# Optimization experiments

Measured on AMD Instinct MI355X. Metric: run time of the kernel, lower is better.

## Reference

```python
import jax, jax.numpy as jnp
import numpy as np

NEG_SLOPE = 0.2
LN_EPS = 1e-5


def setup_inputs() -> dict:
    key = jax.random.key(0)
    k1, k2, k3, k4 = jax.random.split(key, 4)
    N, E, Din, Dout = 50000, 1000000, 64, 64
    h = jax.random.normal(k1, (N, Din), dtype=jnp.float32)
    edge_index = jax.random.randint(k2, (2, E), 0, N, dtype=jnp.int32)
    # Linear(in_dim, out_dim, bias=False): weight [Dout, Din]
    W = jax.random.normal(k3, (Dout, Din), dtype=jnp.float32) / np.sqrt(Din)
    # attention vector a: [1, 2*Dout] (xavier-normal-ish scale)
    a = jax.random.normal(k4, (1, 2 * Dout), dtype=jnp.float32) * 0.1
    ln_gamma = jnp.ones((Dout,), dtype=jnp.float32)
    ln_beta = jnp.zeros((Dout,), dtype=jnp.float32)
    return {"h": h, "edge_index": edge_index, "W": W, "a": a,
            "ln_gamma": ln_gamma, "ln_beta": ln_beta}


def reference(h, edge_index, W, a, ln_gamma, ln_beta):
    N, Dout = h.shape[0], W.shape[0]
    src, dst = edge_index[0], edge_index[1]
    hW = h @ W.T  # [N, Dout]
    # score_e = leakyrelu([h_src || h_dst] . a) = leakyrelu(s1[src] + s2[dst])
    a1, a2 = a[0, :Dout], a[0, Dout:]
    s1 = hW @ a1  # [N]
    s2 = hW @ a2  # [N]
    e = jax.nn.leaky_relu(s1[src] + s2[dst], NEG_SLOPE)  # [E]
    # softmax grouped by source node (segment softmax), numerically stable
    m = jax.ops.segment_max(e, src, num_segments=N)  # [N]
    ex = jnp.exp(e - m[src])
    denom = jax.ops.segment_sum(ex, src, num_segments=N)  # [N]
    att = ex / denom[src]  # [E]  (dropout: eval mode, identity)
    # scatter-add weighted source features into destination nodes
    msg = att[:, None] * hW[src]  # [E, Dout]
    h_prime = jnp.zeros_like(hW).at[dst].add(msg)
    # residual + LayerNorm
    x = hW + h_prime
    mu = jnp.mean(x, axis=-1, keepdims=True)
    var = jnp.var(x, axis=-1, keepdims=True)
    return (x - mu) * jax.lax.rsqrt(var + LN_EPS) * ln_gamma + ln_beta
```

## Files before the change

### kernel.cpp

```cpp
#include <hip/hip_runtime.h>
#include <hip/hip_bf16.h>

#define NEG_SLOPE 0.2f
#define LN_EPS 1e-5f
#define D 64
#define BSH 6
#define BNODES 64
#define NBMAX 1024
#define BCAP 1792
#define SSH 8
#define NSBMAX 256
#define SCAP 6144
#define OVFCAP 65536

typedef unsigned long long u64;
typedef unsigned int u32;
typedef unsigned short u16;

__device__ __forceinline__ u16 f2bf(float f) {
    u32 u = __float_as_uint(f);
    return (u16)((u + 0x7FFFu + ((u >> 16) & 1u)) >> 16);
}
__device__ __forceinline__ float bf_lo(u32 p) { return __uint_as_float(p << 16); }
__device__ __forceinline__ float bf_hi(u32 p) { return __uint_as_float(p & 0xFFFF0000u); }

__global__ void __launch_bounds__(256, 4)
k_hw_scores(const float* __restrict__ h,
            const float* __restrict__ W,
            const float* __restrict__ a,
            float* __restrict__ hW,
            u16* __restrict__ hWb,
            float* __restrict__ s1,
            float* __restrict__ s2,
            int N) {
    const int lane = threadIdx.x & 63;
    const int wid  = threadIdx.x >> 6;
    const int wavesPerBlock = blockDim.x >> 6;
    const int nWaves = gridDim.x * wavesPerBlock;

    float wcol[D];
    {
        const float4* wr = (const float4*)(W + (size_t)lane * D);
        #pragma unroll
        for (int q = 0; q < D / 4; ++q) {
            float4 w4 = wr[q];
            wcol[q * 4 + 0] = w4.x; wcol[q * 4 + 1] = w4.y;
            wcol[q * 4 + 2] = w4.z; wcol[q * 4 + 3] = w4.w;
        }
    }
    const float a1l = a[lane];
    const float a2l = a[D + lane];

    for (int i = blockIdx.x * wavesPerBlock + wid; i < N; i += nWaves) {
        const int iu = __builtin_amdgcn_readfirstlane(i);
        const float* hr = h + (size_t)iu * D;

        float acc0 = 0.f, acc1 = 0.f, acc2 = 0.f, acc3 = 0.f;
        #pragma unroll
        for (int k = 0; k < D; k += 4) {
            acc0 = fmaf(hr[k + 0], wcol[k + 0], acc0);
            acc1 = fmaf(hr[k + 1], wcol[k + 1], acc1);
            acc2 = fmaf(hr[k + 2], wcol[k + 2], acc2);
            acc3 = fmaf(hr[k + 3], wcol[k + 3], acc3);
        }
        float c = (acc0 + acc1) + (acc2 + acc3);
        hW[(size_t)iu * D + lane] = c;
        hWb[(size_t)iu * D + lane] = f2bf(c);

        float p1 = c * a1l;
        float p2 = c * a2l;
        #pragma unroll
        for (int off = 32; off > 0; off >>= 1) {
            p1 += __shfl_xor(p1, off, 64);
            p2 += __shfl_xor(p2, off, 64);
        }
        if (lane == 0) { s1[iu] = p1; s2[iu] = p2; }
    }
}

__device__ __forceinline__ float edge_ex(float v1, float v2) {
    float x = v1 + v2;
    float e = x > 0.f ? x : NEG_SLOPE * x;
    return expf(fminf(e, 60.f));
}

__global__ void __launch_bounds__(1024)
k_bin(const int* __restrict__ src,
      const int* __restrict__ dst,
      const float* __restrict__ s1,
      const float* __restrict__ s2,
      float* __restrict__ denom,
      int* __restrict__ dcnt_g,
      u32* __restrict__ drecs,
      int* __restrict__ scnt_g,
      u32* __restrict__ srecs,
      u32* __restrict__ ovf_rec,
      int* __restrict__ ovf_dst,
      int* __restrict__ ovf_n,
      int E, int nb, int nsb) {
    const int TPB = 1024, EPT = 4;
    __shared__ u32 recbuf[TPB * EPT];
    __shared__ int lcnt[NBMAX], lo[NBMAX], cc[NBMAX], lbase[NBMAX];

    const int tid = threadIdx.x;
    const int chunk = blockIdx.x * (TPB * EPT);
    const int total = min(E - chunk, TPB * EPT);

    int sv[EPT], dv[EPT];
    const int e0 = chunk + tid * EPT;
    if (e0 + EPT <= E) {
        int4 s4 = *(const int4*)(src + e0);
        int4 d4 = *(const int4*)(dst + e0);
        sv[0] = s4.x; sv[1] = s4.y; sv[2] = s4.z; sv[3] = s4.w;
        dv[0] = d4.x; dv[1] = d4.y; dv[2] = d4.z; dv[3] = d4.w;
    } else {
        #pragma unroll
        for (int j = 0; j < EPT; ++j) {
            int i = e0 + j;
            sv[j] = (i < E) ? src[i] : 0;
            dv[j] = (i < E) ? dst[i] : -1;
        }
    }

    for (int i = tid; i < nb; i += TPB) lcnt[i] = 0;
    __syncthreads();
    #pragma unroll
    for (int j = 0; j < EPT; ++j)
        if (dv[j] >= 0) atomicAdd(&lcnt[dv[j] >> BSH], 1);
    __syncthreads();

    if (tid < nb) lo[tid] = lcnt[tid];
    __syncthreads();
    for (int off = 1; off < nb; off <<= 1) {
        int t = 0;
        if (tid < nb && tid >= off) t = lo[tid - off];
        __syncthreads();
        if (tid < nb) lo[tid] += t;
        __syncthreads();
    }
    if (tid < nb) {
        int e_ = lo[tid] - lcnt[tid];
        lo[tid] = e_; cc[tid] = e_;
        if (lcnt[tid]) lbase[tid] = atomicAdd(&dcnt_g[tid], lcnt[tid]);
    }
    __syncthreads();

    #pragma unroll
    for (int j = 0; j < EPT; ++j) {
        if (dv[j] < 0) continue;
        int b = dv[j] >> BSH;
        u32 rec = (u32)sv[j] | ((u32)(dv[j] & (BNODES - 1)) << 16) | ((u32)b << 22);
        recbuf[atomicAdd(&cc[b], 1)] = rec;
    }
    __syncthreads();

    for (int i = tid; i < total; i += TPB) {
        u32 rec = recbuf[i];
        int b = rec >> 22;
        int r = lbase[b] + (i - lo[b]);
        if (r < BCAP) {
            drecs[(size_t)b * BCAP + r] = rec;
        } else {
            int o = atomicAdd(ovf_n, 1);
            if (o < OVFCAP) {
                ovf_rec[o] = rec;
                ovf_dst[o] = (b << BSH) | ((rec >> 16) & (BNODES - 1));
            }
        }
    }
    __syncthreads();

    for (int i = tid; i < nsb; i += TPB) lcnt[i] = 0;
    __syncthreads();
    #pragma unroll
    for (int j = 0; j < EPT; ++j)
        if (dv[j] >= 0) atomicAdd(&lcnt[sv[j] >> SSH], 1);
    __syncthreads();

    if (tid < nsb) lo[tid] = lcnt[tid];
    __syncthreads();
    for (int off = 1; off < nsb; off <<= 1) {
        int t = 0;
        if (tid < nsb && tid >= off) t = lo[tid - off];
        __syncthreads();
        if (tid < nsb) lo[tid] += t;
        __syncthreads();
    }
    if (tid < nsb) {
        int e_ = lo[tid] - lcnt[tid];
        lo[tid] = e_; cc[tid] = e_;
        if (lcnt[tid]) lbase[tid] = atomicAdd(&scnt_g[tid], lcnt[tid]);
    }
    __syncthreads();

    #pragma unroll
    for (int j = 0; j < EPT; ++j) {
        if (dv[j] < 0) continue;
        int b = sv[j] >> SSH;
        u32 rec = (u32)sv[j] | ((u32)dv[j] << 16);
        recbuf[atomicAdd(&cc[b], 1)] = rec;
    }
    __syncthreads();

    for (int i = tid; i < total; i += TPB) {
        u32 rec = recbuf[i];
        int s = rec & 0xFFFF;
        int b = s >> SSH;
        int r = lbase[b] + (i - lo[b]);
        if (r < SCAP) {
            srecs[(size_t)b * SCAP + r] = rec;
        } else {
            atomicAdd(&denom[s], edge_ex(s1[s], s2[rec >> 16]));
        }
    }
}

__global__ void __launch_bounds__(512)
k_denom(const u32* __restrict__ srecs,
        const int* __restrict__ scnt_g,
        const float* __restrict__ s1,
        const float* __restrict__ s2,
        float* __restrict__ denom,
        int N) {
    __shared__ float acc[256];
    const int b = blockIdx.x;
    const int tid = threadIdx.x;
    if (tid < 256) acc[tid] = 0.f;
    __syncthreads();

    const int total = min(scnt_g[b], SCAP);
    const u32* base = srecs + (size_t)b * SCAP;
    for (int i = tid; i < total; i += 512) {
        u32 r = base[i];
        int s = r & 0xFFFF;
        int d = r >> 16;
        atomicAdd(&acc[s & 255], edge_ex(s1[s], s2[d]));
    }
    __syncthreads();

    if (tid < 256) {
        int g = (b << SSH) + tid;
        if (g < N) denom[g] += acc[tid];
    }
}

__global__ void __launch_bounds__(512)
k_bucket_agg(const u32* __restrict__ drecs,
             const int* __restrict__ dcnt_g,
             const float* __restrict__ s1,
             const float* __restrict__ s2,
             const float* __restrict__ denom,
             const float* __restrict__ hW,
             const u16* __restrict__ hWb,
             const float* __restrict__ gamma,
             const float* __restrict__ beta,
             const u32* __restrict__ ovf_rec,
             const int* __restrict__ ovf_dst,
             const int* __restrict__ ovf_n_p,
             float* __restrict__ out,
             int N) {
    __shared__ u64 ro[BCAP];
    __shared__ float s2l[BNODES];
    __shared__ int hh[BNODES], oo[BNODES], cc[BNODES];

    const int b    = blockIdx.x;
    const int tid  = threadIdx.x;
    const int lane = tid & 63;
    const int wid  = tid >> 6;
    const int g    = lane >> 4;
    const int li   = lane & 15;
    const int node0 = b << BSH;
    const int nn    = min(BNODES, N - node0);
    const int total = min(dcnt_g[b], BCAP);

    if (tid < nn) s2l[tid] = s2[node0 + tid];
    if (tid < BNODES) hh[tid] = 0;
    __syncthreads();

    u64 rr[4]; bool valid[4];
    const u32* base = drecs + (size_t)b * BCAP;
    #pragma unroll
    for (int q = 0; q < 4; ++q) {
        int idx = tid + q * 512;
        valid[q] = idx < total;
        u32 r = valid[q] ? base[idx] : 0u;
        if (valid[q]) {
            int s  = r & 0xFFFF;
            int dl = (r >> 16) & (BNODES - 1);
            float att = edge_ex(s1[s], s2l[dl]) / denom[s];
            rr[q] = ((u64)__float_as_uint(att) << 32) | (u64)r;
            atomicAdd(&hh[dl], 1);
        } else rr[q] = 0;
    }
    __syncthreads();

    if (tid < BNODES) oo[tid] = hh[tid];
    __syncthreads();
    for (int off = 1; off < BNODES; off <<= 1) {
        int t = 0;
        if (tid < BNODES && tid >= off) t = oo[tid - off];
        __syncthreads();
        if (tid < BNODES) oo[tid] += t;
        __syncthreads();
    }
    if (tid < BNODES) { int e_ = oo[tid] - hh[tid]; oo[tid] = e_; cc[tid] = e_; }
    __syncthreads();

    #pragma unroll
    for (int q = 0; q < 4; ++q) if (valid[q])
        ro[atomicAdd(&cc[((u32)rr[q] >> 16) & (BNODES - 1)], 1)] = rr[q];
    __syncthreads();

    int ovn = *ovf_n_p;
    if (ovn > OVFCAP) ovn = OVFCAP;

    #pragma unroll
    for (int k = 0; k < 8; ++k) {
        int nl = (wid << 3) + k;
        if (nl >= nn) break;
        int beg = oo[nl], end = cc[nl];

        float ax = 0.f, ay = 0.f, az = 0.f, aw = 0.f;
        for (int p = beg; p < end; p += 16) {
            float at0 = 0.f, at1 = 0.f, at2 = 0.f, at3 = 0.f;
            int s0 = 0, s1i = 0, s2i = 0, s3 = 0;
            int i0 = p + g, i1 = p + 4 + g, i2 = p + 8 + g, i3 = p + 12 + g;
            if (i0 < end) { u64 r2 = ro[i0]; s0  = (u32)r2 & 0xFFFF; at0 = __uint_as_float((u32)(r2 >> 32)); }
            if (i1 < end) { u64 r2 = ro[i1]; s1i = (u32)r2 & 0xFFFF; at1 = __uint_as_float((u32)(r2 >> 32)); }
            if (i2 < end) { u64 r2 = ro[i2]; s2i = (u32)r2 & 0xFFFF; at2 = __uint_as_float((u32)(r2 >> 32)); }
            if (i3 < end) { u64 r2 = ro[i3]; s3  = (u32)r2 & 0xFFFF; at3 = __uint_as_float((u32)(r2 >> 32)); }
            const uint2 v0 = *(const uint2*)(hWb + (size_t)s0  * D + li * 4);
            const uint2 v1 = *(const uint2*)(hWb + (size_t)s1i * D + li * 4);
            const uint2 v2 = *(const uint2*)(hWb + (size_t)s2i * D + li * 4);
            const uint2 v3 = *(const uint2*)(hWb + (size_t)s3  * D + li * 4);
            ax = fmaf(at0, bf_lo(v0.x), ax); ay = fmaf(at0, bf_hi(v0.x), ay);
            az = fmaf(at0, bf_lo(v0.y), az); aw = fmaf(at0, bf_hi(v0.y), aw);
            ax = fmaf(at1, bf_lo(v1.x), ax); ay = fmaf(at1, bf_hi(v1.x), ay);
            az = fmaf(at1, bf_lo(v1.y), az); aw = fmaf(at1, bf_hi(v1.y), aw);
            ax = fmaf(at2, bf_lo(v2.x), ax); ay = fmaf(at2, bf_hi(v2.x), ay);
            az = fmaf(at2, bf_lo(v2.y), az); aw = fmaf(at2, bf_hi(v2.y), aw);
            ax = fmaf(at3, bf_lo(v3.x), ax); ay = fmaf(at3, bf_hi(v3.x), ay);
            az = fmaf(at3, bf_lo(v3.y), az); aw = fmaf(at3, bf_hi(v3.y), aw);
        }

        for (int r = 0; r < ovn; ++r) {
            if (ovf_dst[r] != node0 + nl) continue;
            if (g == 0) {
                u32 r2 = ovf_rec[r];
                int s = r2 & 0xFFFF;
                float att = edge_ex(s1[s], s2l[nl]) / denom[s];
                const uint2 v = *(const uint2*)(hWb + (size_t)s * D + li * 4);
                ax = fmaf(att, bf_lo(v.x), ax); ay = fmaf(att, bf_hi(v.x), ay);
                az = fmaf(att, bf_lo(v.y), az); aw = fmaf(att, bf_hi(v.y), aw);
            }
        }

        ax += __shfl_xor(ax, 16, 64); ax += __shfl_xor(ax, 32, 64);
        ay += __shfl_xor(ay, 16, 64); ay += __shfl_xor(ay, 32, 64);
        az += __shfl_xor(az, 16, 64); az += __shfl_xor(az, 32, 64);
        aw += __shfl_xor(aw, 16, 64); aw += __shfl_xor(aw, 32, 64);

        const float4 hv = *(const float4*)(hW + (size_t)(node0 + nl) * D + li * 4);
        float x0 = hv.x + ax, x1 = hv.y + ay, x2 = hv.z + az, x3 = hv.w + aw;

        float sm = x0 + x1 + x2 + x3;
        sm += __shfl_xor(sm, 1, 64); sm += __shfl_xor(sm, 2, 64);
        sm += __shfl_xor(sm, 4, 64); sm += __shfl_xor(sm, 8, 64);
        float mu = sm * (1.f / D);
        float d0 = x0 - mu, d1 = x1 - mu, d2 = x2 - mu, d3 = x3 - mu;
        float vv = d0 * d0 + d1 * d1 + d2 * d2 + d3 * d3;
        vv += __shfl_xor(vv, 1, 64); vv += __shfl_xor(vv, 2, 64);
        vv += __shfl_xor(vv, 4, 64); vv += __shfl_xor(vv, 8, 64);
        float inv = rsqrtf(vv * (1.f / D) + LN_EPS);

        if (g == 0) {
            const float4 gm = *(const float4*)(gamma + li * 4);
            const float4 bt = *(const float4*)(beta + li * 4);
            float4 o;
            o.x = d0 * inv * gm.x + bt.x;
            o.y = d1 * inv * gm.y + bt.y;
            o.z = d2 * inv * gm.z + bt.z;
            o.w = d3 * inv * gm.w + bt.w;
            *(float4*)(out + (size_t)(node0 + nl) * D + li * 4) = o;
        }
    }
}

static inline size_t align256(size_t x) { return (x + 255) & ~size_t(255); }

extern "C" void kernel_launch(void* const* d_in, const int* in_sizes, int n_in,
                              void* d_out, int out_size, void* d_ws, size_t ws_size,
                              hipStream_t stream) {
    const float* h    = (const float*)d_in[0];
    const int*   ei   = (const int*)d_in[1];
    const float* W    = (const float*)d_in[2];
    const float* a    = (const float*)d_in[3];
    const float* lng  = (const float*)d_in[4];
    const float* lnb  = (const float*)d_in[5];
    float* out = (float*)d_out;

    const int N = in_sizes[0] / D;
    const int E = in_sizes[1] / 2;
    const int* src = ei;
    const int* dst = ei + E;
    const int nb  = (N + BNODES - 1) >> BSH;
    const int nsb = (N + 255) >> SSH;

    char* ws = (char*)d_ws;
    size_t off = 0;
    float* hW      = (float*)(ws + off); off += align256(sizeof(float) * (size_t)N * D);
    u16*   hWb     = (u16*)  (ws + off); off += align256(sizeof(u16) * (size_t)N * D);
    float* s1      = (float*)(ws + off); off += align256(sizeof(float) * (size_t)N);
    float* s2      = (float*)(ws + off); off += align256(sizeof(float) * (size_t)N);
    u32*   drecs   = (u32*)  (ws + off); off += align256(sizeof(u32) * (size_t)nb * BCAP);
    u32*   srecs   = (u32*)  (ws + off); off += align256(sizeof(u32) * (size_t)nsb * SCAP);
    u32*   ovf_rec = (u32*)  (ws + off); off += align256(sizeof(u32) * (size_t)OVFCAP);
    int*   ovf_dst = (int*)  (ws + off); off += align256(sizeof(int) * (size_t)OVFCAP);
    size_t zero_off = off;
    float* denom   = (float*)(ws + off); off += align256(sizeof(float) * (size_t)N);
    int*   dcnt_g  = (int*)  (ws + off); off += align256(sizeof(int) * (size_t)NBMAX);
    int*   scnt_g  = (int*)  (ws + off); off += align256(sizeof(int) * (size_t)NSBMAX);
    int*   ovf_n   = (int*)  (ws + off); off += align256(sizeof(int));
    size_t zero_bytes = off - zero_off;

    hipMemsetAsync(ws + zero_off, 0, zero_bytes, stream);

    k_hw_scores<<<dim3(1024), dim3(256), 0, stream>>>(h, W, a, hW, hWb, s1, s2, N);

    k_bin<<<dim3((E + 4095) / 4096), dim3(1024), 0, stream>>>(
        src, dst, s1, s2, denom, dcnt_g, drecs, scnt_g, srecs,
        ovf_rec, ovf_dst, ovf_n, E, nb, nsb);

    k_denom<<<dim3(nsb), dim3(512), 0, stream>>>(srecs, scnt_g, s1, s2, denom, N);

    k_bucket_agg<<<dim3(nb), dim3(512), 0, stream>>>(
        drecs, dcnt_g, s1, s2, denom, hW, hWb, lng, lnb,
        ovf_rec, ovf_dst, ovf_n, out, N);
}
```

Before: 163.8 us.

## Fuse projection and edge binning into one kernel with block-role split

Merges the hW/score projection kernel and the edge binning kernel into a single launch, where the first blocks bin edges and the remaining 200 blocks compute hW and scores concurrently. Because binning no longer has s1/s2 available, source-bucket overflow edges are written to a new overflow list that k_denom scans, instead of being atomically added into denom. k_denom now writes denom directly. This removes a kernel boundary and overlaps the compute-light projection with the atomic-heavy binning. In exchange, the projection blocks run with 1024 threads and hold a 64-float register array, which limits occupancy, and every k_denom block scans the whole overflow list.

Result: no change. 165.0 us (+0.7%).

```diff
diff --git a/kernel.cpp b/kernel.cpp
--- a/kernel.cpp
+++ b/kernel.cpp
@@ -24,60 +24,6 @@
 __device__ __forceinline__ float bf_lo(u32 p) { return __uint_as_float(p << 16); }
 __device__ __forceinline__ float bf_hi(u32 p) { return __uint_as_float(p & 0xFFFF0000u); }
 
-__global__ void __launch_bounds__(256, 4)
-k_hw_scores(const float* __restrict__ h,
-            const float* __restrict__ W,
-            const float* __restrict__ a,
-            float* __restrict__ hW,
-            u16* __restrict__ hWb,
-            float* __restrict__ s1,
-            float* __restrict__ s2,
-            int N) {
-    const int lane = threadIdx.x & 63;
-    const int wid  = threadIdx.x >> 6;
-    const int wavesPerBlock = blockDim.x >> 6;
-    const int nWaves = gridDim.x * wavesPerBlock;
-
-    float wcol[D];
-    {
-        const float4* wr = (const float4*)(W + (size_t)lane * D);
-        #pragma unroll
-        for (int q = 0; q < D / 4; ++q) {
-            float4 w4 = wr[q];
-            wcol[q * 4 + 0] = w4.x; wcol[q * 4 + 1] = w4.y;
-            wcol[q * 4 + 2] = w4.z; wcol[q * 4 + 3] = w4.w;
-        }
-    }
-    const float a1l = a[lane];
-    const float a2l = a[D + lane];
-
-    for (int i = blockIdx.x * wavesPerBlock + wid; i < N; i += nWaves) {
-        const int iu = __builtin_amdgcn_readfirstlane(i);
-        const float* hr = h + (size_t)iu * D;
-
-        float acc0 = 0.f, acc1 = 0.f, acc2 = 0.f, acc3 = 0.f;
-        #pragma unroll
-        for (int k = 0; k < D; k += 4) {
-            acc0 = fmaf(hr[k + 0], wcol[k + 0], acc0);
-            acc1 = fmaf(hr[k + 1], wcol[k + 1], acc1);
-            acc2 = fmaf(hr[k + 2], wcol[k + 2], acc2);
-            acc3 = fmaf(hr[k + 3], wcol[k + 3], acc3);
-        }
-        float c = (acc0 + acc1) + (acc2 + acc3);
-        hW[(size_t)iu * D + lane] = c;
-        hWb[(size_t)iu * D + lane] = f2bf(c);
-
-        float p1 = c * a1l;
-        float p2 = c * a2l;
-        #pragma unroll
-        for (int off = 32; off > 0; off >>= 1) {
-            p1 += __shfl_xor(p1, off, 64);
-            p2 += __shfl_xor(p2, off, 64);
-        }
-        if (lane == 0) { s1[iu] = p1; s2[iu] = p2; }
-    }
-}
-
 __device__ __forceinline__ float edge_ex(float v1, float v2) {
     float x = v1 + v2;
     float e = x > 0.f ? x : NEG_SLOPE * x;
@@ -85,132 +31,186 @@
 }
 
 __global__ void __launch_bounds__(1024)
-k_bin(const int* __restrict__ src,
-      const int* __restrict__ dst,
-      const float* __restrict__ s1,
-      const float* __restrict__ s2,
-      float* __restrict__ denom,
-      int* __restrict__ dcnt_g,
-      u32* __restrict__ drecs,
-      int* __restrict__ scnt_g,
-      u32* __restrict__ srecs,
-      u32* __restrict__ ovf_rec,
-      int* __restrict__ ovf_dst,
-      int* __restrict__ ovf_n,
-      int E, int nb, int nsb) {
+k_hw_bin(const float* __restrict__ h,
+         const float* __restrict__ W,
+         const float* __restrict__ a,
+         float* __restrict__ hW,
+         u16* __restrict__ hWb,
+         float* __restrict__ s1,
+         float* __restrict__ s2,
+         const int* __restrict__ src,
+         const int* __restrict__ dst,
+         int* __restrict__ dcnt_g,
+         u32* __restrict__ drecs,
+         int* __restrict__ scnt_g,
+         u32* __restrict__ srecs,
+         u32* __restrict__ ovf_rec,
+         int* __restrict__ ovf_dst,
+         int* __restrict__ ovf_n,
+         u32* __restrict__ sovf_rec,
+         int* __restrict__ sovf_n,
+         int N, int E, int nb, int nsb, int nbin) {
     const int TPB = 1024, EPT = 4;
     __shared__ u32 recbuf[TPB * EPT];
     __shared__ int lcnt[NBMAX], lo[NBMAX], cc[NBMAX], lbase[NBMAX];
 
     const int tid = threadIdx.x;
-    const int chunk = blockIdx.x * (TPB * EPT);
-    const int total = min(E - chunk, TPB * EPT);
-
-    int sv[EPT], dv[EPT];
-    const int e0 = chunk + tid * EPT;
-    if (e0 + EPT <= E) {
-        int4 s4 = *(const int4*)(src + e0);
-        int4 d4 = *(const int4*)(dst + e0);
-        sv[0] = s4.x; sv[1] = s4.y; sv[2] = s4.z; sv[3] = s4.w;
-        dv[0] = d4.x; dv[1] = d4.y; dv[2] = d4.z; dv[3] = d4.w;
-    } else {
+
+    if ((int)blockIdx.x < nbin) {
+        const int chunk = blockIdx.x * (TPB * EPT);
+        const int total = min(E - chunk, TPB * EPT);
+
+        int sv[EPT], dv[EPT];
+        const int e0 = chunk + tid * EPT;
+        if (e0 + EPT <= E) {
+            int4 s4 = *(const int4*)(src + e0);
+            int4 d4 = *(const int4*)(dst + e0);
+            sv[0] = s4.x; sv[1] = s4.y; sv[2] = s4.z; sv[3] = s4.w;
+            dv[0] = d4.x; dv[1] = d4.y; dv[2] = d4.z; dv[3] = d4.w;
+        } else {
+            #pragma unroll
+            for (int j = 0; j < EPT; ++j) {
+                int i = e0 + j;
+                sv[j] = (i < E) ? src[i] : 0;
+                dv[j] = (i < E) ? dst[i] : -1;
+            }
+        }
+
+        for (int i = tid; i < nb; i += TPB) lcnt[i] = 0;
+        __syncthreads();
+        #pragma unroll
+        for (int j = 0; j < EPT; ++j)
+            if (dv[j] >= 0) atomicAdd(&lcnt[dv[j] >> BSH], 1);
+        __syncthreads();
+
+        if (tid < nb) lo[tid] = lcnt[tid];
+        __syncthreads();
+        for (int off = 1; off < nb; off <<= 1) {
+            int t = 0;
+            if (tid < nb && tid >= off) t = lo[tid - off];
+            __syncthreads();
+            if (tid < nb) lo[tid] += t;
+            __syncthreads();
+        }
+        if (tid < nb) {
+            int e_ = lo[tid] - lcnt[tid];
+            lo[tid] = e_; cc[tid] = e_;
+            if (lcnt[tid]) lbase[tid] = atomicAdd(&dcnt_g[tid], lcnt[tid]);
+        }
+        __syncthreads();
+
         #pragma unroll
         for (int j = 0; j < EPT; ++j) {
-            int i = e0 + j;
-            sv[j] = (i < E) ? src[i] : 0;
-            dv[j] = (i < E) ? dst[i] : -1;
-        }
-    }
-
-    for (int i = tid; i < nb; i += TPB) lcnt[i] = 0;
-    __syncthreads();
-    #pragma unroll
-    for (int j = 0; j < EPT; ++j)
-        if (dv[j] >= 0) atomicAdd(&lcnt[dv[j] >> BSH], 1);
-    __syncthreads();
-
-    if (tid < nb) lo[tid] = lcnt[tid];
-    __syncthreads();
-    for (int off = 1; off < nb; off <<= 1) {
-        int t = 0;
-        if (tid < nb && tid >= off) t = lo[tid - off];
-        __syncthreads();
-        if (tid < nb) lo[tid] += t;
-        __syncthreads();
-    }
-    if (tid < nb) {
-        int e_ = lo[tid] - lcnt[tid];
-        lo[tid] = e_; cc[tid] = e_;
-        if (lcnt[tid]) lbase[tid] = atomicAdd(&dcnt_g[tid], lcnt[tid]);
-    }
-    __syncthreads();
-
-    #pragma unroll
-    for (int j = 0; j < EPT; ++j) {
-        if (dv[j] < 0) continue;
-        int b = dv[j] >> BSH;
-        u32 rec = (u32)sv[j] | ((u32)(dv[j] & (BNODES - 1)) << 16) | ((u32)b << 22);
-        recbuf[atomicAdd(&cc[b], 1)] = rec;
-    }
-    __syncthreads();
-
-    for (int i = tid; i < total; i += TPB) {
-        u32 rec = recbuf[i];
-        int b = rec >> 22;
-        int r = lbase[b] + (i - lo[b]);
-        if (r < BCAP) {
-            drecs[(size_t)b * BCAP + r] = rec;
-        } else {
-            int o = atomicAdd(ovf_n, 1);
-            if (o < OVFCAP) {
-                ovf_rec[o] = rec;
-                ovf_dst[o] = (b << BSH) | ((rec >> 16) & (BNODES - 1));
-            }
-        }
-    }
-    __syncthreads();
-
-    for (int i = tid; i < nsb; i += TPB) lcnt[i] = 0;
-    __syncthreads();
-    #pragma unroll
-    for (int j = 0; j < EPT; ++j)
-        if (dv[j] >= 0) atomicAdd(&lcnt[sv[j] >> SSH], 1);
-    __syncthreads();
-
-    if (tid < nsb) lo[tid] = lcnt[tid];
-    __syncthreads();
-    for (int off = 1; off < nsb; off <<= 1) {
-        int t = 0;
-        if (tid < nsb && tid >= off) t = lo[tid - off];
-        __syncthreads();
-        if (tid < nsb) lo[tid] += t;
-        __syncthreads();
-    }
-    if (tid < nsb) {
-        int e_ = lo[tid] - lcnt[tid];
-        lo[tid] = e_; cc[tid] = e_;
-        if (lcnt[tid]) lbase[tid] = atomicAdd(&scnt_g[tid], lcnt[tid]);
-    }
-    __syncthreads();
-
-    #pragma unroll
-    for (int j = 0; j < EPT; ++j) {
-        if (dv[j] < 0) continue;
-        int b = sv[j] >> SSH;
-        u32 rec = (u32)sv[j] | ((u32)dv[j] << 16);
-        recbuf[atomicAdd(&cc[b], 1)] = rec;
-    }
-    __syncthreads();
-
-    for (int i = tid; i < total; i += TPB) {
-        u32 rec = recbuf[i];
-        int s = rec & 0xFFFF;
-        int b = s >> SSH;
-        int r = lbase[b] + (i - lo[b]);
-        if (r < SCAP) {
-            srecs[(size_t)b * SCAP + r] = rec;
-        } else {
-            atomicAdd(&denom[s], edge_ex(s1[s], s2[rec >> 16]));
+            if (dv[j] < 0) continue;
+            int b = dv[j] >> BSH;
+            u32 rec = (u32)sv[j] | ((u32)(dv[j] & (BNODES - 1)) << 16) | ((u32)b << 22);
+            recbuf[atomicAdd(&cc[b], 1)] = rec;
+        }
+        __syncthreads();
+
+        for (int i = tid; i < total; i += TPB) {
+            u32 rec = recbuf[i];
+            int b = rec >> 22;
+            int r = lbase[b] + (i - lo[b]);
+            if (r < BCAP) {
+                drecs[(size_t)b * BCAP + r] = rec;
+            } else {
+                int o = atomicAdd(ovf_n, 1);
+                if (o < OVFCAP) {
+                    ovf_rec[o] = rec;
+                    ovf_dst[o] = (b << BSH) | ((rec >> 16) & (BNODES - 1));
+                }
+            }
+        }
+        __syncthreads();
+
+        for (int i = tid; i < nsb; i += TPB) lcnt[i] = 0;
+        __syncthreads();
+        #pragma unroll
+        for (int j = 0; j < EPT; ++j)
+            if (dv[j] >= 0) atomicAdd(&lcnt[sv[j] >> SSH], 1);
+        __syncthreads();
+
+        if (tid < nsb) lo[tid] = lcnt[tid];
+        __syncthreads();
+        for (int off = 1; off < nsb; off <<= 1) {
+            int t = 0;
+            if (tid < nsb && tid >= off) t = lo[tid - off];
+            __syncthreads();
+            if (tid < nsb) lo[tid] += t;
+            __syncthreads();
+        }
+        if (tid < nsb) {
+            int e_ = lo[tid] - lcnt[tid];
+            lo[tid] = e_; cc[tid] = e_;
+            if (lcnt[tid]) lbase[tid] = atomicAdd(&scnt_g[tid], lcnt[tid]);
+        }
+        __syncthreads();
+
+        #pragma unroll
+        for (int j = 0; j < EPT; ++j) {
+            if (dv[j] < 0) continue;
+            int b = sv[j] >> SSH;
+            u32 rec = (u32)sv[j] | ((u32)dv[j] << 16);
+            recbuf[atomicAdd(&cc[b], 1)] = rec;
+        }
+        __syncthreads();
+
+        for (int i = tid; i < total; i += TPB) {
+            u32 rec = recbuf[i];
+            int s = rec & 0xFFFF;
+            int b = s >> SSH;
+            int r = lbase[b] + (i - lo[b]);
+            if (r < SCAP) {
+                srecs[(size_t)b * SCAP + r] = rec;
+            } else {
+                int o = atomicAdd(sovf_n, 1);
+                if (o < OVFCAP) sovf_rec[o] = rec;
+            }
+        }
+    } else {
+        const int lane = tid & 63;
+        const int wid  = tid >> 6;
+        const int hwBlocks = (int)gridDim.x - nbin;
+        const int nWaves = hwBlocks * 16;
+
+        float wcol[D];
+        {
+            const float4* wr = (const float4*)(W + (size_t)lane * D);
+            #pragma unroll
+            for (int q = 0; q < D / 4; ++q) {
+                float4 w4 = wr[q];
+                wcol[q * 4 + 0] = w4.x; wcol[q * 4 + 1] = w4.y;
+                wcol[q * 4 + 2] = w4.z; wcol[q * 4 + 3] = w4.w;
+            }
+        }
+        const float a1l = a[lane];
+        const float a2l = a[D + lane];
+
+        for (int i = ((int)blockIdx.x - nbin) * 16 + wid; i < N; i += nWaves) {
+            const int iu = __builtin_amdgcn_readfirstlane(i);
+            const float* hr = h + (size_t)iu * D;
+
+            float acc0 = 0.f, acc1 = 0.f, acc2 = 0.f, acc3 = 0.f;
+            #pragma unroll
+            for (int k = 0; k < D; k += 4) {
+                acc0 = fmaf(hr[k + 0], wcol[k + 0], acc0);
+                acc1 = fmaf(hr[k + 1], wcol[k + 1], acc1);
+                acc2 = fmaf(hr[k + 2], wcol[k + 2], acc2);
+                acc3 = fmaf(hr[k + 3], wcol[k + 3], acc3);
+            }
+            float c = (acc0 + acc1) + (acc2 + acc3);
+            hW[(size_t)iu * D + lane] = c;
+            hWb[(size_t)iu * D + lane] = f2bf(c);
+
+            float p1 = c * a1l;
+            float p2 = c * a2l;
+            #pragma unroll
+            for (int off = 32; off > 0; off >>= 1) {
+                p1 += __shfl_xor(p1, off, 64);
+                p2 += __shfl_xor(p2, off, 64);
+            }
+            if (lane == 0) { s1[iu] = p1; s2[iu] = p2; }
         }
     }
 }
@@ -220,6 +220,8 @@
         const int* __restrict__ scnt_g,
         const float* __restrict__ s1,
         const float* __restrict__ s2,
+        const u32* __restrict__ sovf_rec,
+        const int* __restrict__ sovf_n_p,
         float* __restrict__ denom,
         int N) {
     __shared__ float acc[256];
@@ -236,11 +238,20 @@
         int d = r >> 16;
         atomicAdd(&acc[s & 255], edge_ex(s1[s], s2[d]));
     }
+
+    int sn = *sovf_n_p;
+    if (sn > OVFCAP) sn = OVFCAP;
+    for (int r = tid; r < sn; r += 512) {
+        u32 rec = sovf_rec[r];
+        int s = rec & 0xFFFF;
+        if ((s >> SSH) == b)
+            atomicAdd(&acc[s & 255], edge_ex(s1[s], s2[rec >> 16]));
+    }
     __syncthreads();
 
     if (tid < 256) {
         int g = (b << SSH) + tid;
-        if (g < N) denom[g] += acc[tid];
+        if (g < N) denom[g] = acc[tid];
     }
 }
 
@@ -288,7 +299,7 @@
             int s  = r & 0xFFFF;
             int dl = (r >> 16) & (BNODES - 1);
             float att = edge_ex(s1[s], s2l[dl]) / denom[s];
-            rr[q] = ((u64)__float_as_uint(att) << 32) | (u64)r;
+            rr[q] = ((u64)__float_as_uint(att) << 32) | (u64)(r & 0x3FFFFFu);
             atomicAdd(&hh[dl], 1);
         } else rr[q] = 0;
     }
@@ -405,6 +416,8 @@
     const int* dst = ei + E;
     const int nb  = (N + BNODES - 1) >> BSH;
     const int nsb = (N + 255) >> SSH;
+    const int nbin = (E + 4095) / 4096;
+    const int nhw  = 200;
 
     char* ws = (char*)d_ws;
     size_t off = 0;
@@ -416,22 +429,25 @@
     u32*   srecs   = (u32*)  (ws + off); off += align256(sizeof(u32) * (size_t)nsb * SCAP);
     u32*   ovf_rec = (u32*)  (ws + off); off += align256(sizeof(u32) * (size_t)OVFCAP);
     int*   ovf_dst = (int*)  (ws + off); off += align256(sizeof(int) * (size_t)OVFCAP);
+    u32*   sovf_rec= (u32*)  (ws + off); off += align256(sizeof(u32) * (size_t)OVFCAP);
     size_t zero_off = off;
     float* denom   = (float*)(ws + off); off += align256(sizeof(float) * (size_t)N);
     int*   dcnt_g  = (int*)  (ws + off); off += align256(sizeof(int) * (size_t)NBMAX);
     int*   scnt_g  = (int*)  (ws + off); off += align256(sizeof(int) * (size_t)NSBMAX);
     int*   ovf_n   = (int*)  (ws + off); off += align256(sizeof(int));
+    int*   sovf_n  = (int*)  (ws + off); off += align256(sizeof(int));
     size_t zero_bytes = off - zero_off;
 
     hipMemsetAsync(ws + zero_off, 0, zero_bytes, stream);
 
-    k_hw_scores<<<dim3(1024), dim3(256), 0, stream>>>(h, W, a, hW, hWb, s1, s2, N);
-
-    k_bin<<<dim3((E + 4095) / 4096), dim3(1024), 0, stream>>>(
-        src, dst, s1, s2, denom, dcnt_g, drecs, scnt_g, srecs,
-        ovf_rec, ovf_dst, ovf_n, E, nb, nsb);
-
-    k_denom<<<dim3(nsb), dim3(512), 0, stream>>>(srecs, scnt_g, s1, s2, denom, N);
+    k_hw_bin<<<dim3(nbin + nhw), dim3(1024), 0, stream>>>(
+        h, W, a, hW, hWb, s1, s2, src, dst,
+        dcnt_g, drecs, scnt_g, srecs,
+        ovf_rec, ovf_dst, ovf_n, sovf_rec, sovf_n,
+        N, E, nb, nsb, nbin);
+
+    k_denom<<<dim3(nsb), dim3(512), 0, stream>>>(
+        srecs, scnt_g, s1, s2, sovf_rec, sovf_n, denom, N);
 
     k_bucket_agg<<<dim3(nb), dim3(512), 0, stream>>>(
         drecs, dcnt_g, s1, s2, denom, hW, hWb, lng, lnb,
```
